# Kernel optimization log

Hardware: AMD Instinct MI355X
Metric: run time of the kernel (lower is better)

## Reference

```python
import jax, jax.numpy as jnp
import numpy as np

B, T, H = 256, 2048, 128
LSTM_IN = [24, 128, 128]


def _xavier(key, fan_out, fan_in):
    std = (2.0 / (fan_in + fan_out)) ** 0.5
    return jax.random.normal(key, (fan_out, fan_in), jnp.float32) * std


def setup_inputs() -> dict:
    key = jax.random.key(0)
    ks = jax.random.split(key, 32)
    inp = {}
    inp['scent'] = jax.random.normal(ks[0], (B, T, 3), jnp.float32)
    # fc1: Linear(3,12) + ReLU + Linear(12,24) + ReLU, xavier weights, zero bias
    inp['W1'] = _xavier(ks[1], 12, 3); inp['b1'] = jnp.zeros((12,), jnp.float32)
    inp['W2'] = _xavier(ks[2], 24, 12); inp['b2'] = jnp.zeros((24,), jnp.float32)
    # 3-layer LSTM, PyTorch default init: uniform(-1/sqrt(H), 1/sqrt(H)) for all params
    k = 1.0 / np.sqrt(H)
    for l in range(3):
        d = LSTM_IN[l]
        inp[f'Wih{l}'] = jax.random.uniform(ks[4 + 4 * l], (4 * H, d), jnp.float32, -k, k)
        inp[f'Whh{l}'] = jax.random.uniform(ks[5 + 4 * l], (4 * H, H), jnp.float32, -k, k)
        inp[f'bih{l}'] = jax.random.uniform(ks[6 + 4 * l], (4 * H,), jnp.float32, -k, k)
        inp[f'bhh{l}'] = jax.random.uniform(ks[7 + 4 * l], (4 * H,), jnp.float32, -k, k)
    # fc2: Linear(128,64) + ReLU + Linear(64,32) + ReLU
    inp['Wf1'] = _xavier(ks[20], 64, 128); inp['bf1'] = jnp.zeros((64,), jnp.float32)
    inp['Wf2'] = _xavier(ks[21], 32, 64); inp['bf2'] = jnp.zeros((32,), jnp.float32)
    return inp


def _lstm_layer(x, Wih, Whh, bih, bhh):
    # x: [T, B, D] -> ys: [T, B, H]; PyTorch gate order i, f, g, o
    gx = jnp.einsum('tbd,gd->tbg', x, Wih) + bih + bhh  # [T, B, 4H]

    def step(carry, g_t):
        h, c = carry
        gates = g_t + h @ Whh.T
        i, f, g, o = jnp.split(gates, 4, axis=-1)
        c = jax.nn.sigmoid(f) * c + jax.nn.sigmoid(i) * jnp.tanh(g)
        h = jax.nn.sigmoid(o) * jnp.tanh(c)
        return (h, c), h

    h0 = jnp.zeros((x.shape[1], H), x.dtype)
    (hT, cT), ys = jax.lax.scan(step, (h0, h0), gx)
    return ys, hT, cT


def reference(scent, W1, b1, W2, b2,
              Wih0, Whh0, bih0, bhh0,
              Wih1, Whh1, bih1, bhh1,
              Wih2, Whh2, bih2, bhh2,
              Wf1, bf1, Wf2, bf2):
    # fc1 (pointwise over B*T)
    x = jax.nn.relu(scent @ W1.T + b1)
    x = jax.nn.relu(x @ W2.T + b2)          # [B, T, 24]
    x = jnp.transpose(x, (1, 0, 2))          # [T, B, 24] seq-first
    hs, cs = [], []
    for Wih, Whh, bih, bhh in ((Wih0, Whh0, bih0, bhh0),
                               (Wih1, Whh1, bih1, bhh1),
                               (Wih2, Whh2, bih2, bhh2)):
        x, hT, cT = _lstm_layer(x, Wih, Whh, bih, bhh)
        hs.append(hT); cs.append(cT)
    h = jnp.stack(hs)                        # [3, B, H]
    c = jnp.stack(cs)                        # [3, B, H]
    y = jnp.transpose(x, (1, 0, 2))          # [B, T, H]
    y = jax.nn.relu(y @ Wf1.T + bf1)
    out = jax.nn.relu(y @ Wf2.T + bf2)       # [B, T, 32]
    return out, h, c
```

## Files before the change

kernel.cpp:

```cpp
#include <hip/hip_runtime.h>

#define B 256
#define T 2048
#define HDIM 128
#define CH 256
#define NCHUNK (T / CH)

typedef _Float16 f16;
typedef _Float16 h2 __attribute__((ext_vector_type(2)));
typedef _Float16 f16x8 __attribute__((ext_vector_type(8)));
typedef float f32x4 __attribute__((ext_vector_type(4)));

__device__ __forceinline__ float dot2(h2 a, h2 b, float c) {
#if __has_builtin(__builtin_amdgcn_fdot2)
    return __builtin_amdgcn_fdot2(a, b, c, false);
#else
    return c + (float)a[0] * (float)b[0] + (float)a[1] * (float)b[1];
#endif
}

__device__ __forceinline__ float rcp_(float x) {
#if __has_builtin(__builtin_amdgcn_rcpf)
    return __builtin_amdgcn_rcpf(x);
#else
    return 1.0f / x;
#endif
}
__device__ __forceinline__ float sigm(float x) { return rcp_(1.0f + __expf(-x)); }
__device__ __forceinline__ float tanh_(float x) {
    float e = __expf(-2.0f * fabsf(x));
    float t = fmaf(2.0f, rcp_(1.0f + e), -1.0f);
    return copysignf(t, x);
}

__device__ __forceinline__ float dpp_x1(float x) {
#if __has_builtin(__builtin_amdgcn_update_dpp)
    union { float f; int i; } u, r;
    u.f = x;
    r.i = __builtin_amdgcn_update_dpp(0, u.i, 0xB1, 0xF, 0xF, true);
    return r.f;
#else
    return __shfl_xor(x, 1);
#endif
}
__device__ __forceinline__ float dpp_x2(float x) {
#if __has_builtin(__builtin_amdgcn_update_dpp)
    union { float f; int i; } u, r;
    u.f = x;
    r.i = __builtin_amdgcn_update_dpp(0, u.i, 0x4E, 0xF, 0xF, true);
    return r.f;
#else
    return __shfl_xor(x, 2);
#endif
}

__device__ __forceinline__ void bar() {
    asm volatile("s_waitcnt lgkmcnt(0)" ::: "memory");
    __builtin_amdgcn_s_barrier();
}

__global__ __launch_bounds__(256) void fc1_kernel(
    const float* __restrict__ scent,
    const float* __restrict__ W1, const float* __restrict__ b1,
    const float* __restrict__ W2, const float* __restrict__ b2,
    f16* __restrict__ x1) {
    int r = blockIdx.x * 256 + threadIdx.x;
    int b = r >> 11, t = r & 2047;
    float s0 = scent[r * 3], s1 = scent[r * 3 + 1], s2 = scent[r * 3 + 2];
    float a[12];
#pragma unroll
    for (int i = 0; i < 12; i++) {
        float v = W1[i * 3] * s0 + W1[i * 3 + 1] * s1 + W1[i * 3 + 2] * s2 + b1[i];
        a[i] = fmaxf(v, 0.f);
    }
    union { f16 o[32]; uint4 u[4]; } U;
#pragma unroll
    for (int j = 0; j < 24; j++) {
        float v = b2[j];
#pragma unroll
        for (int i = 0; i < 12; i++) v = fmaf(W2[j * 12 + i], a[i], v);
        U.o[j] = (f16)fmaxf(v, 0.f);
    }
#pragma unroll
    for (int j = 24; j < 32; j++) U.o[j] = (f16)0.f;
    uint4* d4 = (uint4*)(x1 + ((size_t)t * B + b) * 32);
#pragma unroll
    for (int i = 0; i < 4; i++) d4[i] = U.u[i];
}

__global__ __launch_bounds__(256) void pack_kernel(const float* __restrict__ w,
                                                   unsigned int* __restrict__ o) {
    int i = blockIdx.x * 256 + threadIdx.x;
    if (i < 4096) {
        union { h2 h; unsigned int u; } U;
        U.h[0] = (f16)w[2 * i];
        U.h[1] = (f16)w[2 * i + 1];
        o[i] = U.u;
    }
}

template <int KIN, int KREAL, int SP>
__global__ __launch_bounds__(256) void gx_gemm(
    const f16* __restrict__ x,
    const float* __restrict__ Wih,
    const float* __restrict__ bih, const float* __restrict__ bhh,
    f16* __restrict__ gx,
    int t0) {
    constexpr int KF = KIN / 32;
    __shared__ __align__(16) f16 Alds[64 * SP];
    const int tid = threadIdx.x;
    const int mb = blockIdx.x, nb = blockIdx.y;
    const int l = tid & 63, wv = tid >> 6;
    const int lc = l & 15, lg = l >> 4;

    const f16* xrow = x + ((size_t)t0 * B + (size_t)mb * 64) * KIN;
    if (KIN == 128) {
#pragma unroll
        for (int it = 0; it < 4; it++) {
            int row = it * 16 + (tid >> 4), cc = tid & 15;
            uint4 v = *(const uint4*)(xrow + (size_t)row * KIN + cc * 8);
            *(uint4*)(&Alds[row * SP + cc * 8]) = v;
        }
    } else {
        int row = tid >> 2, cc = tid & 3;
        uint4 v = *(const uint4*)(xrow + (size_t)row * KIN + cc * 8);
        *(uint4*)(&Alds[row * SP + cc * 8]) = v;
    }

    const int gbase = nb * 128 + (wv & 1) * 64;
    const int rbase = (wv >> 1) * 32;
    f16x8 bf[4][KF];
    float bias4[4];
#pragma unroll
    for (int gt = 0; gt < 4; gt++) {
        int g = gbase + gt * 16 + lc;
        bias4[gt] = bih[g] + bhh[g];
#pragma unroll
        for (int kf = 0; kf < KF; kf++) {
            f16x8 v;
#pragma unroll
            for (int j = 0; j < 8; j++) {
                int k = kf * 32 + lg * 8 + j;
                v[j] = (k < KREAL) ? (f16)Wih[(size_t)g * KREAL + k] : (f16)0.f;
            }
            bf[gt][kf] = v;
        }
    }
    __syncthreads();

    f32x4 acc[2][4] = {};
#pragma unroll
    for (int kf = 0; kf < KF; kf++) {
#pragma unroll
        for (int rt = 0; rt < 2; rt++) {
            f16x8 af = *(const f16x8*)(&Alds[(rbase + rt * 16 + lc) * SP + kf * 32 + lg * 8]);
#pragma unroll
            for (int gt = 0; gt < 4; gt++)
                acc[rt][gt] = __builtin_amdgcn_mfma_f32_16x16x32_f16(af, bf[gt][kf], acc[rt][gt], 0, 0, 0);
        }
    }
#pragma unroll
    for (int rt = 0; rt < 2; rt++)
#pragma unroll
        for (int gt = 0; gt < 4; gt++)
#pragma unroll
            for (int q = 0; q < 4; q++) {
                int rr = mb * 64 + rbase + rt * 16 + lg * 4 + q;
                int gg = gbase + gt * 16 + lc;
                gx[(size_t)rr * 512 + gg] = (f16)(acc[rt][gt][q] + bias4[gt]);
            }
}

__global__ __attribute__((amdgpu_flat_work_group_size(512, 512), amdgpu_waves_per_eu(2, 2)))
void lstm_rec(
    const f16* __restrict__ gx,
    const float* __restrict__ Whh,
    f16* __restrict__ y,
    float* __restrict__ hS, float* __restrict__ cS,
    int t0, int init) {
    __shared__ __align__(16) f16 hbuf[2][HDIM];
    const int tid = threadIdx.x, bb = blockIdx.x;
    const int j = tid >> 2, q = tid & 3;

    h2 wh[4][16];
#pragma unroll
    for (int gi = 0; gi < 4; gi++) {
        const float* wr = Whh + (size_t)(gi * 128 + j) * HDIM + 32 * q;
#pragma unroll
        for (int kk = 0; kk < 16; kk++) {
            h2 p; p[0] = (f16)wr[2 * kk]; p[1] = (f16)wr[2 * kk + 1];
            wh[gi][kk] = p;
        }
    }
    float c = 0.f;
    {
        float hv = 0.f;
        if (!init) { hv = hS[bb * HDIM + j]; c = cS[bb * HDIM + j]; }
        if (q == 0) hbuf[0][j] = (f16)hv;
    }
    const ushort* gp = (const ushort*)gx + (size_t)bb * 512 + q * 128 + j;
    ushort gxr[8];
#pragma unroll
    for (int jj = 0; jj < 8; jj++) gxr[jj] = gp[(size_t)jj * (B * 512)];
    f16* yp = y + ((size_t)t0 * B + bb) * HDIM + j;
    __syncthreads();

    float hh = 0.f;
    for (int w8 = 0; w8 < CH / 8; w8++) {
#pragma unroll
        for (int jj = 0; jj < 8; jj++) {
            const int t = w8 * 8 + jj;
            const int p = t & 1;
            union { ushort u; f16 h; } GU; GU.u = gxr[jj];
            float gxv = (float)GU.h;
            int tn = t + 8; if (tn > CH - 1) tn = CH - 1;
            gxr[jj] = gp[(size_t)tn * (B * 512)];

            union { uint4 u[4]; h2 h[16]; } S;
            {
                const uint4* kp = (const uint4*)(&hbuf[p][32 * q]);
                S.u[0] = kp[0]; S.u[1] = kp[1]; S.u[2] = kp[2]; S.u[3] = kp[3];
            }
            float acc[4];
#pragma unroll
            for (int gi = 0; gi < 4; gi++) acc[gi] = (q == gi) ? gxv : 0.f;
#pragma unroll
            for (int kk = 0; kk < 16; kk++) {
#pragma unroll
                for (int gi = 0; gi < 4; gi++) acc[gi] = dot2(wh[gi][kk], S.h[kk], acc[gi]);
            }
#pragma unroll
            for (int gi = 0; gi < 4; gi++) {
                acc[gi] += dpp_x1(acc[gi]);
                acc[gi] += dpp_x2(acc[gi]);
            }
            float gi_ = sigm(acc[0]), gf_ = sigm(acc[1]);
            float gg_ = tanh_(acc[2]), go_ = sigm(acc[3]);
            c = gf_ * c + gi_ * gg_;
            hh = go_ * tanh_(c);
            if (q == 0) {
                hbuf[p ^ 1][j] = (f16)hh;
                *yp = (f16)hh;
            }
            yp += (size_t)B * HDIM;
            bar();
        }
    }
    if (q == 0) {
        hS[bb * HDIM + j] = hh;
        cS[bb * HDIM + j] = c;
    }
}

__global__ __launch_bounds__(256) void fc2_kernel(
    const f16* __restrict__ yin,
    const unsigned int* __restrict__ w1,
    const float* __restrict__ bf1,
    const float* __restrict__ Wf2,
    const float* __restrict__ bf2,
    float* __restrict__ out) {
    int r = blockIdx.x * 256 + threadIdx.x;
    union { uint4 u4[16]; h2 h[64]; } Y;
    {
        const uint4* yr4 = (const uint4*)(yin + (size_t)r * 128);
#pragma unroll
        for (int i = 0; i < 16; i++) Y.u4[i] = yr4[i];
    }
    float acc2[32];
#pragma unroll
    for (int i = 0; i < 32; i++) acc2[i] = 0.f;

    for (int cO = 0; cO < 64; cO++) {
        float a0 = bf1[cO], a1 = 0.f, a2 = 0.f, a3 = 0.f;
#pragma unroll
        for (int kk = 0; kk < 64; kk += 4) {
            union { unsigned int u; h2 h; } W0, W1x, W2x, W3;
            W0.u = w1[cO * 64 + kk];      a0 = dot2(W0.h,  Y.h[kk],     a0);
            W1x.u = w1[cO * 64 + kk + 1]; a1 = dot2(W1x.h, Y.h[kk + 1], a1);
            W2x.u = w1[cO * 64 + kk + 2]; a2 = dot2(W2x.h, Y.h[kk + 2], a2);
            W3.u = w1[cO * 64 + kk + 3];  a3 = dot2(W3.h,  Y.h[kk + 3], a3);
        }
        float a = fmaxf((a0 + a1) + (a2 + a3), 0.f);
#pragma unroll
        for (int c2 = 0; c2 < 32; c2++) acc2[c2] = fmaf(a, Wf2[c2 * 64 + cO], acc2[c2]);
    }
    float* orow = out + ((size_t)(r & 255) * T + (r >> 8)) * 32;
#pragma unroll
    for (int c2 = 0; c2 < 32; c2++) orow[c2] = fmaxf(acc2[c2] + bf2[c2], 0.f);
}

extern "C" void kernel_launch(void* const* d_in, const int* in_sizes, int n_in,
                              void* d_out, int out_size, void* d_ws, size_t ws_size,
                              hipStream_t stream) {
    const float* scent = (const float*)d_in[0];
    const float* W1 = (const float*)d_in[1];
    const float* b1 = (const float*)d_in[2];
    const float* W2 = (const float*)d_in[3];
    const float* b2 = (const float*)d_in[4];
    const float* Wih[3] = {(const float*)d_in[5], (const float*)d_in[9], (const float*)d_in[13]};
    const float* Whh[3] = {(const float*)d_in[6], (const float*)d_in[10], (const float*)d_in[14]};
    const float* bihp[3] = {(const float*)d_in[7], (const float*)d_in[11], (const float*)d_in[15]};
    const float* bhhp[3] = {(const float*)d_in[8], (const float*)d_in[12], (const float*)d_in[16]};
    const float* Wf1 = (const float*)d_in[17];
    const float* bf1 = (const float*)d_in[18];
    const float* Wf2 = (const float*)d_in[19];
    const float* bf2 = (const float*)d_in[20];

    const size_t o_x1 = 0;
    const size_t o_y  = 33554432;
    const size_t o_gx = o_y + 134217728;
    const size_t o_w1 = o_gx + 67108864;
    const size_t need = o_w1 + 16384;
    if (ws_size < need) return;

    char* ws = (char*)d_ws;
    f16* x1 = (f16*)(ws + o_x1);
    f16* yb = (f16*)(ws + o_y);
    f16* gxb = (f16*)(ws + o_gx);
    unsigned int* w1p = (unsigned int*)(ws + o_w1);

    float* out = (float*)d_out;
    float* hO = out + (size_t)B * T * 32;
    float* cO = hO + 3 * B * HDIM;

    pack_kernel<<<16, 256, 0, stream>>>(Wf1, w1p);
    fc1_kernel<<<(B * T) / 256, 256, 0, stream>>>(scent, W1, b1, W2, b2, x1);

    dim3 ggrid(CH * B / 64, 4);
    for (int l = 0; l < 3; l++) {
        float* hS = hO + (size_t)l * B * HDIM;
        float* cS = cO + (size_t)l * B * HDIM;
        for (int ch = 0; ch < NCHUNK; ch++) {
            int t0 = ch * CH;
            if (l == 0)
                gx_gemm<32, 24, 40><<<ggrid, 256, 0, stream>>>(x1, Wih[0], bihp[0], bhhp[0], gxb, t0);
            else
                gx_gemm<128, 128, 144><<<ggrid, 256, 0, stream>>>(yb, Wih[l], bihp[l], bhhp[l], gxb, t0);
            lstm_rec<<<B, 512, 0, stream>>>(gxb, Whh[l], yb, hS, cS, t0, ch == 0 ? 1 : 0);
        }
    }
    fc2_kernel<<<(B * T) / 256, 256, 0, stream>>>(yb, w1p, bf1, Wf2, bf2, out);
}
```

Before: 5.177 ms.

## Fuse input-gate GEMM into a persistent cooperative LSTM layer kernel

Replaces the per-chunk gx_gemm and lstm_rec launches with one cooperative kernel per layer. Each warp computes its slice of the input-gate GEMM between recurrence chunks, with grid-wide syncs and double-buffered gate storage, and the chunk size is halved. This removes the many kernel launches and inter-kernel gaps. In exchange, each warp reloads fp32 Wih from global memory inside the fused GEMM, the GEMM is not overlapped with the recurrence, and grid.sync overhead is added. It also simplifies tanh by dropping the abs/copysign form.

```diff
diff --git a/kernel.cpp b/kernel.cpp
--- a/kernel.cpp
+++ b/kernel.cpp
@@ -1,9 +1,10 @@
 #include <hip/hip_runtime.h>
+#include <hip/hip_cooperative_groups.h>
 
 #define B 256
 #define T 2048
 #define HDIM 128
-#define CH 256
+#define CH 128
 #define NCHUNK (T / CH)
 
 typedef _Float16 f16;
@@ -27,10 +28,8 @@
 #endif
 }
 __device__ __forceinline__ float sigm(float x) { return rcp_(1.0f + __expf(-x)); }
-__device__ __forceinline__ float tanh_(float x) {
-    float e = __expf(-2.0f * fabsf(x));
-    float t = fmaf(2.0f, rcp_(1.0f + e), -1.0f);
-    return copysignf(t, x);
+__device__ __forceinline__ float tanh2(float x) {
+    return fmaf(2.0f, rcp_(1.0f + __expf(-2.0f * x)), -1.0f);
 }
 
 __device__ __forceinline__ float dpp_x1(float x) {
@@ -99,88 +98,25 @@
     }
 }
 
-template <int KIN, int KREAL, int SP>
-__global__ __launch_bounds__(256) void gx_gemm(
-    const f16* __restrict__ x,
+template <int KF, int KREAL>
+__global__ __attribute__((amdgpu_flat_work_group_size(512, 512), amdgpu_waves_per_eu(2, 2)))
+void lstm_layer(
+    const f16* x,
     const float* __restrict__ Wih,
+    const float* __restrict__ Whh,
     const float* __restrict__ bih, const float* __restrict__ bhh,
-    f16* __restrict__ gx,
-    int t0) {
-    constexpr int KF = KIN / 32;
-    __shared__ __align__(16) f16 Alds[64 * SP];
-    const int tid = threadIdx.x;
-    const int mb = blockIdx.x, nb = blockIdx.y;
-    const int l = tid & 63, wv = tid >> 6;
-    const int lc = l & 15, lg = l >> 4;
-
-    const f16* xrow = x + ((size_t)t0 * B + (size_t)mb * 64) * KIN;
-    if (KIN == 128) {
-#pragma unroll
-        for (int it = 0; it < 4; it++) {
-            int row = it * 16 + (tid >> 4), cc = tid & 15;
-            uint4 v = *(const uint4*)(xrow + (size_t)row * KIN + cc * 8);
-            *(uint4*)(&Alds[row * SP + cc * 8]) = v;
-        }
-    } else {
-        int row = tid >> 2, cc = tid & 3;
-        uint4 v = *(const uint4*)(xrow + (size_t)row * KIN + cc * 8);
-        *(uint4*)(&Alds[row * SP + cc * 8]) = v;
-    }
-
-    const int gbase = nb * 128 + (wv & 1) * 64;
-    const int rbase = (wv >> 1) * 32;
-    f16x8 bf[4][KF];
-    float bias4[4];
-#pragma unroll
-    for (int gt = 0; gt < 4; gt++) {
-        int g = gbase + gt * 16 + lc;
-        bias4[gt] = bih[g] + bhh[g];
-#pragma unroll
-        for (int kf = 0; kf < KF; kf++) {
-            f16x8 v;
-#pragma unroll
-            for (int j = 0; j < 8; j++) {
-                int k = kf * 32 + lg * 8 + j;
-                v[j] = (k < KREAL) ? (f16)Wih[(size_t)g * KREAL + k] : (f16)0.f;
-            }
-            bf[gt][kf] = v;
-        }
-    }
-    __syncthreads();
-
-    f32x4 acc[2][4] = {};
-#pragma unroll
-    for (int kf = 0; kf < KF; kf++) {
-#pragma unroll
-        for (int rt = 0; rt < 2; rt++) {
-            f16x8 af = *(const f16x8*)(&Alds[(rbase + rt * 16 + lc) * SP + kf * 32 + lg * 8]);
-#pragma unroll
-            for (int gt = 0; gt < 4; gt++)
-                acc[rt][gt] = __builtin_amdgcn_mfma_f32_16x16x32_f16(af, bf[gt][kf], acc[rt][gt], 0, 0, 0);
-        }
-    }
-#pragma unroll
-    for (int rt = 0; rt < 2; rt++)
-#pragma unroll
-        for (int gt = 0; gt < 4; gt++)
-#pragma unroll
-            for (int q = 0; q < 4; q++) {
-                int rr = mb * 64 + rbase + rt * 16 + lg * 4 + q;
-                int gg = gbase + gt * 16 + lc;
-                gx[(size_t)rr * 512 + gg] = (f16)(acc[rt][gt][q] + bias4[gt]);
-            }
-}
-
-__global__ __attribute__((amdgpu_flat_work_group_size(512, 512), amdgpu_waves_per_eu(2, 2)))
-void lstm_rec(
-    const f16* __restrict__ gx,
-    const float* __restrict__ Whh,
-    f16* __restrict__ y,
-    float* __restrict__ hS, float* __restrict__ cS,
-    int t0, int init) {
+    f16* y,
+    float* __restrict__ hT, float* __restrict__ cT,
+    f16* __restrict__ gxA, f16* __restrict__ gxB) {
+    constexpr int KIN = KF * 32;
+    cooperative_groups::grid_group grid = cooperative_groups::this_grid();
     __shared__ __align__(16) f16 hbuf[2][HDIM];
+
     const int tid = threadIdx.x, bb = blockIdx.x;
     const int j = tid >> 2, q = tid & 3;
+    const int wv = tid >> 6, l = tid & 63;
+    const int lc = l & 15, lg = l >> 4;
+    const int wid = bb * 8 + wv;
 
     h2 wh[4][16];
 #pragma unroll
@@ -192,63 +128,100 @@
             wh[gi][kk] = p;
         }
     }
-    float c = 0.f;
-    {
-        float hv = 0.f;
-        if (!init) { hv = hS[bb * HDIM + j]; c = cS[bb * HDIM + j]; }
-        if (q == 0) hbuf[0][j] = (f16)hv;
-    }
-    const ushort* gp = (const ushort*)gx + (size_t)bb * 512 + q * 128 + j;
-    ushort gxr[8];
-#pragma unroll
-    for (int jj = 0; jj < 8; jj++) gxr[jj] = gp[(size_t)jj * (B * 512)];
-    f16* yp = y + ((size_t)t0 * B + bb) * HDIM + j;
-    __syncthreads();
-
-    float hh = 0.f;
-    for (int w8 = 0; w8 < CH / 8; w8++) {
-#pragma unroll
-        for (int jj = 0; jj < 8; jj++) {
-            const int t = w8 * 8 + jj;
-            const int p = t & 1;
-            union { ushort u; f16 h; } GU; GU.u = gxr[jj];
-            float gxv = (float)GU.h;
-            int tn = t + 8; if (tn > CH - 1) tn = CH - 1;
-            gxr[jj] = gp[(size_t)tn * (B * 512)];
-
-            union { uint4 u[4]; h2 h[16]; } S;
-            {
-                const uint4* kp = (const uint4*)(&hbuf[p][32 * q]);
-                S.u[0] = kp[0]; S.u[1] = kp[1]; S.u[2] = kp[2]; S.u[3] = kp[3];
+    float c = 0.f, hh = 0.f;
+    if (q == 0) hbuf[0][j] = (f16)0.f;
+
+    f16* gxbuf0 = gxA;
+    f16* gxbuf1 = gxB;
+
+    auto do_gemm = [&](int ch) {
+        f16* gxo = ((ch & 1) ? gxbuf1 : gxbuf0) + (size_t)wid * 16 * 512;
+        const size_t rowbase = (size_t)ch * CH * B + (size_t)wid * 16;
+        f16x8 af[KF];
+#pragma unroll
+        for (int kf = 0; kf < KF; kf++)
+            af[kf] = *(const f16x8*)(x + (rowbase + lc) * KIN + kf * 32 + lg * 8);
+        for (int gt = 0; gt < 32; gt++) {
+            int g = gt * 16 + lc;
+            float bs = bih[g] + bhh[g];
+            f32x4 a = {bs, bs, bs, bs};
+#pragma unroll
+            for (int kf = 0; kf < KF; kf++) {
+                const float* wr = Wih + (size_t)g * KREAL + kf * 32 + lg * 8;
+                f16x8 bf;
+#pragma unroll
+                for (int e = 0; e < 8; e++) {
+                    int k = kf * 32 + lg * 8 + e;
+                    bf[e] = (k < KREAL) ? (f16)wr[e] : (f16)0.f;
+                }
+                a = __builtin_amdgcn_mfma_f32_16x16x32_f16(af[kf], bf, a, 0, 0, 0);
             }
-            float acc[4];
-#pragma unroll
-            for (int gi = 0; gi < 4; gi++) acc[gi] = (q == gi) ? gxv : 0.f;
-#pragma unroll
-            for (int kk = 0; kk < 16; kk++) {
-#pragma unroll
-                for (int gi = 0; gi < 4; gi++) acc[gi] = dot2(wh[gi][kk], S.h[kk], acc[gi]);
-            }
-#pragma unroll
-            for (int gi = 0; gi < 4; gi++) {
-                acc[gi] += dpp_x1(acc[gi]);
-                acc[gi] += dpp_x2(acc[gi]);
-            }
-            float gi_ = sigm(acc[0]), gf_ = sigm(acc[1]);
-            float gg_ = tanh_(acc[2]), go_ = sigm(acc[3]);
-            c = gf_ * c + gi_ * gg_;
-            hh = go_ * tanh_(c);
-            if (q == 0) {
-                hbuf[p ^ 1][j] = (f16)hh;
-                *yp = (f16)hh;
-            }
-            yp += (size_t)B * HDIM;
-            bar();
-        }
-    }
+#pragma unroll
+            for (int qq = 0; qq < 4; qq++)
+                gxo[(size_t)(4 * lg + qq) * 512 + g] = (f16)a[qq];
+        }
+    };
+
+    do_gemm(0);
+    grid.sync();
+
+#define RSTEP(TT, JJ, RF)                                                      \
+    {                                                                           \
+        const int p_ = (TT) & 1;                                                \
+        union { ushort u; f16 h; } GU_; GU_.u = gxr[JJ];                        \
+        float gxv = (float)GU_.h;                                               \
+        if (RF) { gxr[JJ] = *gq; gq += B * 512; }                               \
+        union { uint4 u[4]; h2 h[16]; } S_;                                     \
+        {                                                                       \
+            const uint4* kp = (const uint4*)(&hbuf[p_][32 * q]);                \
+            S_.u[0] = kp[0]; S_.u[1] = kp[1]; S_.u[2] = kp[2]; S_.u[3] = kp[3]; \
+        }                                                                       \
+        float a0 = (q == 0) ? gxv : 0.f, a1 = (q == 1) ? gxv : 0.f;             \
+        float a2 = (q == 2) ? gxv : 0.f, a3 = (q == 3) ? gxv : 0.f;             \
+        _Pragma("unroll")                                                       \
+        for (int kk = 0; kk < 16; kk++) {                                       \
+            a0 = dot2(wh[0][kk], S_.h[kk], a0);                                 \
+            a1 = dot2(wh[1][kk], S_.h[kk], a1);                                 \
+            a2 = dot2(wh[2][kk], S_.h[kk], a2);                                 \
+            a3 = dot2(wh[3][kk], S_.h[kk], a3);                                 \
+        }                                                                       \
+        a0 += dpp_x1(a0); a1 += dpp_x1(a1); a2 += dpp_x1(a2); a3 += dpp_x1(a3); \
+        a0 += dpp_x2(a0); a1 += dpp_x2(a1); a2 += dpp_x2(a2); a3 += dpp_x2(a3); \
+        float gi_ = sigm(a0), gf_ = sigm(a1), gg_ = tanh2(a2), go_ = sigm(a3);  \
+        c = gf_ * c + gi_ * gg_;                                                \
+        hh = go_ * tanh2(c);                                                    \
+        if (q == 0) { hbuf[p_ ^ 1][j] = (f16)hh; *yp = (f16)hh; }               \
+        yp += (size_t)B * HDIM;                                                 \
+        bar();                                                                  \
+    }
+
+    for (int ch = 0; ch < NCHUNK; ch++) {
+        const f16* gxc = (ch & 1) ? gxbuf1 : gxbuf0;
+        const ushort* gp = (const ushort*)gxc + (size_t)bb * 512 + q * 128 + j;
+        ushort gxr[8];
+#pragma unroll
+        for (int jj = 0; jj < 8; jj++) gxr[jj] = gp[(size_t)jj * (B * 512)];
+        const ushort* gq = gp + (size_t)8 * (B * 512);
+        f16* yp = y + ((size_t)ch * CH * B + bb) * HDIM + j;
+
+        for (int w8 = 0; w8 < CH / 8 - 1; w8++) {
+#pragma unroll
+            for (int jj = 0; jj < 8; jj++) RSTEP(w8 * 8 + jj, jj, 1)
+        }
+#pragma unroll
+        for (int jj = 0; jj < 8; jj++) RSTEP(CH - 8 + jj, jj, 0)
+
+        grid.sync();
+        if (ch + 1 < NCHUNK) {
+            do_gemm(ch + 1);
+            grid.sync();
+        }
+    }
+#undef RSTEP
+
     if (q == 0) {
-        hS[bb * HDIM + j] = hh;
-        cS[bb * HDIM + j] = c;
+        hT[(size_t)bb * HDIM + j] = hh;
+        cT[(size_t)bb * HDIM + j] = c;
     }
 }
 
@@ -308,16 +281,17 @@
 
     const size_t o_x1 = 0;
     const size_t o_y  = 33554432;
-    const size_t o_gx = o_y + 134217728;
-    const size_t o_w1 = o_gx + 67108864;
-    const size_t need = o_w1 + 16384;
+    const size_t o_w1 = o_y + 134217728;
+    const size_t o_gx = o_w1 + 16384;
+    const size_t need = o_gx + 67108864;
     if (ws_size < need) return;
 
     char* ws = (char*)d_ws;
     f16* x1 = (f16*)(ws + o_x1);
     f16* yb = (f16*)(ws + o_y);
-    f16* gxb = (f16*)(ws + o_gx);
     unsigned int* w1p = (unsigned int*)(ws + o_w1);
+    f16* gx0 = (f16*)(ws + o_gx);
+    f16* gx1 = gx0 + (size_t)CH * B * 512;
 
     float* out = (float*)d_out;
     float* hO = out + (size_t)B * T * 32;
@@ -326,18 +300,28 @@
     pack_kernel<<<16, 256, 0, stream>>>(Wf1, w1p);
     fc1_kernel<<<(B * T) / 256, 256, 0, stream>>>(scent, W1, b1, W2, b2, x1);
 
-    dim3 ggrid(CH * B / 64, 4);
-    for (int l = 0; l < 3; l++) {
-        float* hS = hO + (size_t)l * B * HDIM;
-        float* cS = cO + (size_t)l * B * HDIM;
-        for (int ch = 0; ch < NCHUNK; ch++) {
-            int t0 = ch * CH;
-            if (l == 0)
-                gx_gemm<32, 24, 40><<<ggrid, 256, 0, stream>>>(x1, Wih[0], bihp[0], bhhp[0], gxb, t0);
-            else
-                gx_gemm<128, 128, 144><<<ggrid, 256, 0, stream>>>(yb, Wih[l], bihp[l], bhhp[l], gxb, t0);
-            lstm_rec<<<B, 512, 0, stream>>>(gxb, Whh[l], yb, hS, cS, t0, ch == 0 ? 1 : 0);
-        }
-    }
+    {
+        void (*k1)(const f16*, const float*, const float*, const float*, const float*,
+                   f16*, float*, float*, f16*, f16*) = lstm_layer<1, 24>;
+        void (*k4)(const f16*, const float*, const float*, const float*, const float*,
+                   f16*, float*, float*, f16*, f16*) = lstm_layer<4, 128>;
+        for (int lyr = 0; lyr < 3; lyr++) {
+            const f16* xl = (lyr == 0) ? (const f16*)x1 : (const f16*)yb;
+            const float* wih = Wih[lyr];
+            const float* whh = Whh[lyr];
+            const float* bi = bihp[lyr];
+            const float* bh = bhhp[lyr];
+            f16* yl = yb;
+            float* hS = hO + (size_t)lyr * B * HDIM;
+            float* cS = cO + (size_t)lyr * B * HDIM;
+            f16* g0 = gx0;
+            f16* g1 = gx1;
+            void* args[] = {(void*)&xl, (void*)&wih, (void*)&whh, (void*)&bi, (void*)&bh,
+                            (void*)&yl, (void*)&hS, (void*)&cS, (void*)&g0, (void*)&g1};
+            hipLaunchCooperativeKernel((lyr == 0) ? (void*)k1 : (void*)k4,
+                                       dim3(B), dim3(512), args, 0, stream);
+        }
+    }
+
     fc2_kernel<<<(B * T) / 256, 256, 0, stream>>>(yb, w1p, bf1, Wf2, bf2, out);
 }
```

After: 8.847 ms. 70.9% more time.
